# Performance work log

Hardware: AMD Instinct MI355X
Metric: run time of the kernel (lower is better)

The kernel has to match this reference:

```python
import jax, jax.numpy as jnp
import numpy as np
from jax import lax

H = 1024
D = 128
T = 64  # n_step + n_middle


def gru_cell(x, h, w_ih, w_hh, b_ih, b_hh):
    # torch.nn.GRUCell gate order: r, z, n
    gi = x @ w_ih.T + b_ih
    gh = h @ w_hh.T + b_hh
    ir, iz, i_n = jnp.split(gi, 3, axis=-1)
    hr, hz, h_n = jnp.split(gh, 3, axis=-1)
    r = jax.nn.sigmoid(ir + hr)
    z = jax.nn.sigmoid(iz + hz)
    n = jnp.tanh(i_n + r * h_n)
    return (1.0 - z) * n + z * h


def decoder(z_seq, z8, n1, w_init, b_init, wi1, wh1, bi1, bh1, wi2, wh2, bi2, bh2, w_out, b_out):
    B = z_seq.shape[0]
    out0 = jnp.zeros((B, D), z_seq.dtype).at[:, -1].set(1.0)
    h0 = z8 @ w_init.T + b_init              # [B, H]
    h1 = jnp.zeros_like(h0)                  # replaced at i == 0
    xs = (jnp.arange(T), jnp.swapaxes(z_seq, 0, 1))  # ([T], [T, B, D])

    def step(carry, x):
        h0, h1, out = carry
        i, z_i = x
        inp = jnp.where(i <= n1 - 1, z_i, out)
        h0n = gru_cell(inp, h0, wi1, wh1, bi1, bh1)
        h1 = jnp.where(i == 0, h0n, h1)
        h1n = gru_cell(h0n, h1, wi2, wh2, bi2, bh2)
        out = h1n @ w_out.T + b_out          # [B, 128]
        return (h0n, h1n, out), out

    _, outs = lax.scan(step, (h0, h1, out0), xs)  # [T, B, 128]
    return jnp.swapaxes(outs[n1 - 1:], 0, 1)      # [B, T-n1+1, 128]


def _p(key, shape):
    return jax.random.normal(key, shape, dtype=jnp.float32) * 0.02


def setup_inputs() -> dict:
    key = jax.random.key(0)
    ks = jax.random.split(key, 32)
    B = 2048
    inp = {
        'zp': jax.random.normal(ks[0], (B, T, D), jnp.float32),
        'zr': jax.random.normal(ks[1], (B, T, D), jnp.float32),
        'zp8': jax.random.normal(ks[2], (B, D), jnp.float32),
        'zr8': jax.random.normal(ks[3], (B, D), jnp.float32),
        'n1': 16,
        'n2': 48,
    }
    # GRU cells 1..4: (w_ih [3H, in], w_hh [3H, H], b_ih [3H], b_hh [3H])
    for j, name in enumerate(['1', '2', '3', '4']):
        in_dim = D if name in ('1', '3') else H
        inp['wi' + name] = _p(ks[4 + 4 * j], (3 * H, in_dim))
        inp['wh' + name] = _p(ks[5 + 4 * j], (3 * H, H))
        inp['bi' + name] = _p(ks[6 + 4 * j], (3 * H,))
        inp['bh' + name] = _p(ks[7 + 4 * j], (3 * H,))
    inp['w_init0'] = _p(ks[20], (H, D)); inp['b_init0'] = _p(ks[21], (H,))
    inp['w_init1'] = _p(ks[22], (H, D)); inp['b_init1'] = _p(ks[23], (H,))
    inp['w_out0'] = _p(ks[24], (D, H)); inp['b_out0'] = _p(ks[25], (D,))
    inp['w_out1'] = _p(ks[26], (D, H)); inp['b_out1'] = _p(ks[27], (D,))
    return inp


def reference(zp, zr, zp8, zr8, n1, n2,
              wi1, wh1, bi1, bh1, wi2, wh2, bi2, bh2,
              wi3, wh3, bi3, bh3, wi4, wh4, bi4, bh4,
              w_init0, b_init0, w_init1, b_init1,
              w_out0, b_out0, w_out1, b_out1):
    z_r = decoder(zr, zr8, n1, w_init0, b_init0, wi1, wh1, bi1, bh1,
                  wi2, wh2, bi2, bh2, w_out0, b_out0)
    z_p = decoder(zp, zp8, n1, w_init1, b_init1, wi3, wh3, bi3, bh3,
                  wi4, wh4, bi4, bh4, w_out1, b_out1)
    return (z_p, z_r)
```

## Files before the change

kernel.cpp:

```cpp
#include <hip/hip_runtime.h>

typedef unsigned short u16;
typedef unsigned int u32;
typedef __attribute__((ext_vector_type(8))) short short8;
typedef __attribute__((ext_vector_type(4))) float f32x4;

#define DEV __device__ __forceinline__

DEV u16 f2bf(float f){
  u32 u = __builtin_bit_cast(u32, f);
  u += 0x7fffu + ((u >> 16) & 1u);
  return (u16)(u >> 16);
}
DEV float sigm(float x){ return 1.f / (1.f + __expf(-x)); }
DEV float tanh_(float x){ return 2.f / (1.f + __expf(-2.f * x)) - 1.f; }

DEV void gl_lds16(const void* g, void* l){
  __builtin_amdgcn_global_load_lds(
      (const __attribute__((address_space(1))) u32*)g,
      (__attribute__((address_space(3))) u32*)l, 16, 0, 0);
}

__global__ void pack_w_kernel(const float* __restrict__ wi, const float* __restrict__ wh,
                              u16* __restrict__ dst, int Ki, int Kh, int nrows){
  const int KT = Ki + Kh;
  const long n = (long)nrows * KT;
  for (long idx = (long)blockIdx.x * blockDim.x + threadIdx.x; idx < n;
       idx += (long)gridDim.x * blockDim.x){
    int r = (int)(idx / KT), c = (int)(idx % KT);
    float v = (c < Ki) ? wi[(long)r * Ki + c] : wh[(long)r * Kh + (c - Ki)];
    dst[idx] = f2bf(v);
  }
}

struct InitA { const float* z8; const float* wini; const float* bini; float* h0f; u16* h0bf; };

__global__ __launch_bounds__(256)
void init_kernel(InitA A0, InitA A1){
  const InitA& a = (blockIdx.z == 0) ? A0 : A1;
  __shared__ float lz[64][128];
  const int tid = threadIdx.x;
  const int rb = blockIdx.x * 64, ub = blockIdx.y * 128;
  {
    const int row = tid >> 2, q = tid & 3;
    const float4* p = (const float4*)(a.z8 + (long)(rb + row) * 128 + q * 32);
    float4* dst = (float4*)&lz[row][q * 32];
    #pragma unroll
    for (int j = 0; j < 8; ++j) dst[j] = p[j];
  }
  __syncthreads();
  const int u = ub + (tid & 127);
  const int rg = tid >> 7;
  float acc[32];
  #pragma unroll
  for (int r = 0; r < 32; ++r) acc[r] = 0.f;
  for (int k = 0; k < 128; k += 4){
    float4 w4 = *(const float4*)&a.wini[(long)u * 128 + k];
    #pragma unroll
    for (int r = 0; r < 32; ++r){
      float4 z4 = *(const float4*)&lz[rg * 32 + r][k];
      acc[r] += w4.x * z4.x + w4.y * z4.y + w4.z * z4.z + w4.w * z4.w;
    }
  }
  const float b = a.bini[u];
  #pragma unroll
  for (int r = 0; r < 32; ++r){
    const long row = rb + rg * 32 + r;
    const float v = acc[r] + b;
    a.h0f[row * 1024 + u] = v;
    a.h0bf[row * 1024 + u] = f2bf(v);
  }
}

struct CellA {
  const u16* W;
  const float* bi; const float* bh;
  const float* afz; const float* afo;
  const u16* ab1; const u16* ab2;
  const float* holdr; float* holdw; u16* hbfw;
};

template<int CELL>
__global__ __launch_bounds__(256, 2)
void cell_kernel(CellA A0, CellA A1, const int* dn1, int step){
  constexpr int KTOT = (CELL == 1) ? 1152 : 2048;
  constexpr int KT = KTOT / 64;
  constexpr int KSPLIT = (CELL == 1) ? 128 : 1024;

  __shared__ u16 lA[128 * 64];
  __shared__ u16 lB[3][32 * 64];

  const CellA& a = (blockIdx.z == 0) ? A0 : A1;
  const int tid = threadIdx.x;
  const int lane = tid & 63;
  const int wv = tid >> 6;
  const int brow = blockIdx.x * 128;
  const int u0 = blockIdx.y * 32;

  f32x4 accR[2][2] = {}; f32x4 accZ[2][2] = {};
  f32x4 accNI[2][2] = {}; f32x4 accNH[2][2] = {};

  const float* fsrc = nullptr; long fstr = 0;
  if constexpr (CELL == 1){
    const int n1v = *dn1;
    if (step < n1v){ fsrc = a.afz; fstr = 64 * 128; }
    else           { fsrc = a.afo; fstr = 128; }
  }

  const int srow = tid >> 3;
  const int sxor8 = ((tid & 7) ^ (srow & 7)) * 8;

  for (int kt = 0; kt < KT; ++kt){
    const int k0 = kt * 64;
    __syncthreads();
    if constexpr (CELL == 1){
      if (k0 < 128){
        const int row = tid >> 1, half = tid & 1;
        const float* p = fsrc + (long)(brow + row) * fstr + k0 + half * 32;
        #pragma unroll
        for (int q = 0; q < 4; ++q){
          float4 x = ((const float4*)p)[2 * q];
          float4 y = ((const float4*)p)[2 * q + 1];
          short8 o;
          o[0] = (short)f2bf(x.x); o[1] = (short)f2bf(x.y);
          o[2] = (short)f2bf(x.z); o[3] = (short)f2bf(x.w);
          o[4] = (short)f2bf(y.x); o[5] = (short)f2bf(y.y);
          o[6] = (short)f2bf(y.z); o[7] = (short)f2bf(y.w);
          const int s = half * 4 + q;
          *(short8*)&lA[row * 64 + ((s ^ (row & 7)) * 8)] = o;
        }
      } else {
        const int kk = k0 - 128;
        #pragma unroll
        for (int j = 0; j < 4; ++j){
          const int row = j * 32 + srow;
          gl_lds16(a.ab1 + (long)(brow + row) * 1024 + kk + sxor8,
                   &lA[(j * 32 + wv * 8) * 64]);
        }
      }
    } else {
      const u16* ab; int kk;
      if (k0 < 1024){ ab = a.ab1; kk = k0; } else { ab = a.ab2; kk = k0 - 1024; }
      #pragma unroll
      for (int j = 0; j < 4; ++j){
        const int row = j * 32 + srow;
        gl_lds16(ab + (long)(brow + row) * 1024 + kk + sxor8,
                 &lA[(j * 32 + wv * 8) * 64]);
      }
    }
    #pragma unroll
    for (int g = 0; g < 3; ++g){
      gl_lds16(a.W + (long)(g * 1024 + u0 + srow) * KTOT + k0 + sxor8,
               &lB[g][wv * 8 * 64]);
    }
    __syncthreads();

    const int l15 = lane & 15;
    const int kq = lane >> 4;
    const int sx = lane & 7;
    #pragma unroll
    for (int ks = 0; ks < 2; ++ks){
      const int soff = (((ks * 4 + kq) ^ sx)) * 8;
      short8 af[2], bR[2], bZ[2], bN[2];
      #pragma unroll
      for (int fr = 0; fr < 2; ++fr)
        af[fr] = *(const short8*)&lA[(wv * 32 + fr * 16 + l15) * 64 + soff];
      #pragma unroll
      for (int fc = 0; fc < 2; ++fc){
        bR[fc] = *(const short8*)&lB[0][(fc * 16 + l15) * 64 + soff];
        bZ[fc] = *(const short8*)&lB[1][(fc * 16 + l15) * 64 + soff];
        bN[fc] = *(const short8*)&lB[2][(fc * 16 + l15) * 64 + soff];
      }
      if (k0 < KSPLIT){
        #pragma unroll
        for (int fr = 0; fr < 2; ++fr)
          #pragma unroll
          for (int fc = 0; fc < 2; ++fc){
            accR[fr][fc] = __builtin_amdgcn_mfma_f32_16x16x32_bf16(af[fr], bR[fc], accR[fr][fc], 0, 0, 0);
            accZ[fr][fc] = __builtin_amdgcn_mfma_f32_16x16x32_bf16(af[fr], bZ[fc], accZ[fr][fc], 0, 0, 0);
            accNI[fr][fc] = __builtin_amdgcn_mfma_f32_16x16x32_bf16(af[fr], bN[fc], accNI[fr][fc], 0, 0, 0);
          }
      } else {
        #pragma unroll
        for (int fr = 0; fr < 2; ++fr)
          #pragma unroll
          for (int fc = 0; fc < 2; ++fc){
            accR[fr][fc] = __builtin_amdgcn_mfma_f32_16x16x32_bf16(af[fr], bR[fc], accR[fr][fc], 0, 0, 0);
            accZ[fr][fc] = __builtin_amdgcn_mfma_f32_16x16x32_bf16(af[fr], bZ[fc], accZ[fr][fc], 0, 0, 0);
            accNH[fr][fc] = __builtin_amdgcn_mfma_f32_16x16x32_bf16(af[fr], bN[fc], accNH[fr][fc], 0, 0, 0);
          }
      }
    }
  }

  const int l15 = lane & 15;
  const int rq = (lane >> 4) * 4;
  #pragma unroll
  for (int fc = 0; fc < 2; ++fc){
    const int u = u0 + fc * 16 + l15;
    const float br = a.bi[u] + a.bh[u];
    const float bz = a.bi[1024 + u] + a.bh[1024 + u];
    const float bni = a.bi[2048 + u];
    const float bnh = a.bh[2048 + u];
    #pragma unroll
    for (int fr = 0; fr < 2; ++fr){
      #pragma unroll
      for (int rg = 0; rg < 4; ++rg){
        const long row = brow + wv * 32 + fr * 16 + rq + rg;
        const float r = sigm(accR[fr][fc][rg] + br);
        const float z = sigm(accZ[fr][fc][rg] + bz);
        const float n = tanh_(accNI[fr][fc][rg] + bni + r * (accNH[fr][fc][rg] + bnh));
        const float hp = a.holdr[row * 1024 + u];
        const float hn = (1.f - z) * n + z * hp;
        a.holdw[row * 1024 + u] = hn;
        a.hbfw[row * 1024 + u] = f2bf(hn);
      }
    }
  }
}

struct OutA { const u16* Ah; const u16* Wo; const float* bo; float* outf; };

__global__ __launch_bounds__(256, 2)
void out_kernel(OutA A0, OutA A1, const int* dn1, int step, float* __restrict__ dout, long outhalf){
  const int n1v = *dn1;
  if (step < n1v - 1) return;
  __shared__ u16 lA[32 * 64];
  __shared__ u16 lB[128 * 64];
  const OutA& a = (blockIdx.z == 0) ? A0 : A1;
  const int tid = threadIdx.x, lane = tid & 63, wv = tid >> 6;
  const int brow = blockIdx.x * 32;
  f32x4 acc[2][2] = {};
  const int srow = tid >> 3;
  const int sxor8 = ((tid & 7) ^ (srow & 7)) * 8;

  for (int kt = 0; kt < 16; ++kt){
    const int k0 = kt * 64;
    __syncthreads();
    gl_lds16(a.Ah + (long)(brow + srow) * 1024 + k0 + sxor8, &lA[wv * 8 * 64]);
    #pragma unroll
    for (int j = 0; j < 4; ++j){
      const int row = j * 32 + srow;
      gl_lds16(a.Wo + (long)row * 1024 + k0 + sxor8, &lB[(j * 32 + wv * 8) * 64]);
    }
    __syncthreads();
    const int l15 = lane & 15, kq = lane >> 4, sx = lane & 7;
    #pragma unroll
    for (int ks = 0; ks < 2; ++ks){
      const int soff = (((ks * 4 + kq) ^ sx)) * 8;
      short8 af[2], bf[2];
      af[0] = *(const short8*)&lA[(l15) * 64 + soff];
      af[1] = *(const short8*)&lA[(16 + l15) * 64 + soff];
      bf[0] = *(const short8*)&lB[(wv * 32 + l15) * 64 + soff];
      bf[1] = *(const short8*)&lB[(wv * 32 + 16 + l15) * 64 + soff];
      #pragma unroll
      for (int fr = 0; fr < 2; ++fr)
        #pragma unroll
        for (int fc = 0; fc < 2; ++fc)
          acc[fr][fc] = __builtin_amdgcn_mfma_f32_16x16x32_bf16(af[fr], bf[fc], acc[fr][fc], 0, 0, 0);
    }
  }
  const int nst = 65 - n1v;
  const int t = step - (n1v - 1);
  const int l15 = lane & 15;
  const int rq = (lane >> 4) * 4;
  #pragma unroll
  for (int fc = 0; fc < 2; ++fc){
    const int u = wv * 32 + fc * 16 + l15;
    const float bo = a.bo[u];
    #pragma unroll
    for (int fr = 0; fr < 2; ++fr){
      #pragma unroll
      for (int rg = 0; rg < 4; ++rg){
        const long row = brow + fr * 16 + rq + rg;
        const float v = acc[fr][fc][rg] + bo;
        a.outf[row * 128 + u] = v;
        dout[(long)blockIdx.z * outhalf + (row * nst + t) * 128 + u] = v;
      }
    }
  }
}

extern "C" void kernel_launch(void* const* d_in, const int* in_sizes, int n_in,
                              void* d_out, int out_size, void* d_ws, size_t ws_size,
                              hipStream_t stream){
  const float* zz[2]   = { (const float*)d_in[0],  (const float*)d_in[1] };
  const float* z8[2]   = { (const float*)d_in[2],  (const float*)d_in[3] };
  const int* dn1       = (const int*)d_in[4];
  const float* wi_c1[2] = { (const float*)d_in[14], (const float*)d_in[6] };
  const float* wh_c1[2] = { (const float*)d_in[15], (const float*)d_in[7] };
  const float* bi_c1[2] = { (const float*)d_in[16], (const float*)d_in[8] };
  const float* bh_c1[2] = { (const float*)d_in[17], (const float*)d_in[9] };
  const float* wi_c2[2] = { (const float*)d_in[18], (const float*)d_in[10] };
  const float* wh_c2[2] = { (const float*)d_in[19], (const float*)d_in[11] };
  const float* bi_c2[2] = { (const float*)d_in[20], (const float*)d_in[12] };
  const float* bh_c2[2] = { (const float*)d_in[21], (const float*)d_in[13] };
  const float* wini[2]  = { (const float*)d_in[24], (const float*)d_in[22] };
  const float* bini[2]  = { (const float*)d_in[25], (const float*)d_in[23] };
  const float* wout[2]  = { (const float*)d_in[28], (const float*)d_in[26] };
  const float* bout[2]  = { (const float*)d_in[29], (const float*)d_in[27] };

  char* p = (char*)d_ws;
  auto alloc = [&](size_t bytes)->char*{
    char* q = p; p += (bytes + 255) & ~(size_t)255; return q;
  };
  u16* W1c[2]; u16* W2c[2]; u16* Woc[2];
  float* h0f[2]; float* h1f[2]; float* outf[2];
  u16* h0bf[2][2]; u16* h1bf[2][2];
  for (int d = 0; d < 2; ++d){
    W1c[d] = (u16*)alloc(3072ULL * 1152 * 2);
    W2c[d] = (u16*)alloc(3072ULL * 2048 * 2);
    Woc[d] = (u16*)alloc(128ULL * 1024 * 2);
    h0f[d] = (float*)alloc(2048ULL * 1024 * 4);
    h1f[d] = (float*)alloc(2048ULL * 1024 * 4);
    outf[d] = (float*)alloc(2048ULL * 128 * 4);
    for (int b = 0; b < 2; ++b){
      h0bf[d][b] = (u16*)alloc(2048ULL * 1024 * 2);
      h1bf[d][b] = (u16*)alloc(2048ULL * 1024 * 2);
    }
  }
  if ((size_t)(p - (char*)d_ws) > ws_size) return;

  for (int d = 0; d < 2; ++d){
    pack_w_kernel<<<dim3(1024), dim3(256), 0, stream>>>(wi_c1[d], wh_c1[d], W1c[d], 128, 1024, 3072);
    pack_w_kernel<<<dim3(1024), dim3(256), 0, stream>>>(wi_c2[d], wh_c2[d], W2c[d], 1024, 1024, 3072);
    pack_w_kernel<<<dim3(64),   dim3(256), 0, stream>>>(wout[d], wout[d], Woc[d], 1024, 0, 128);
  }
  {
    InitA I0{ z8[0], wini[0], bini[0], h0f[0], h0bf[0][0] };
    InitA I1{ z8[1], wini[1], bini[1], h0f[1], h0bf[1][0] };
    init_kernel<<<dim3(32, 8, 2), dim3(256), 0, stream>>>(I0, I1);
  }

  const long outhalf = (long)out_size / 2;

  for (int i = 0; i < 64; ++i){
    const int cur = i & 1, nxt = cur ^ 1;
    CellA c1[2], c2[2];
    for (int d = 0; d < 2; ++d){
      c1[d] = CellA{ W1c[d], bi_c1[d], bh_c1[d],
                     zz[d] + (long)i * 128, outf[d],
                     h0bf[d][cur], nullptr,
                     h0f[d], h0f[d], h0bf[d][nxt] };
      c2[d] = CellA{ W2c[d], bi_c2[d], bh_c2[d],
                     nullptr, nullptr,
                     h0bf[d][nxt], (i == 0) ? h0bf[d][nxt] : h1bf[d][cur],
                     (i == 0) ? h0f[d] : h1f[d], h1f[d], h1bf[d][nxt] };
    }
    cell_kernel<1><<<dim3(16, 32, 2), dim3(256), 0, stream>>>(c1[0], c1[1], dn1, i);
    cell_kernel<2><<<dim3(16, 32, 2), dim3(256), 0, stream>>>(c2[0], c2[1], dn1, i);
    OutA o0{ h1bf[0][nxt], Woc[0], bout[0], outf[0] };
    OutA o1{ h1bf[1][nxt], Woc[1], bout[1], outf[1] };
    out_kernel<<<dim3(64, 1, 2), dim3(256), 0, stream>>>(o0, o1, dn1, i, (float*)d_out, outhalf);
  }
}
```

Measured before the change: 8.247 ms.

## Double-buffer LDS tiles in GRU cell and output GEMM kernels

Both the GRU cell kernel and the output projection kernel now keep two LDS buffers. The next K-tile's global-to-LDS loads are issued before the MFMA work on the current tile, with one barrier per iteration instead of two. This is meant to hide global load latency behind compute. It doubles shared memory use, which may lower occupancy under launch_bounds(256,2), and relies on the async global_load_lds having completed by the time of the barrier.

```diff
diff --git a/kernel.cpp b/kernel.cpp
--- a/kernel.cpp
+++ b/kernel.cpp
@@ -87,8 +87,8 @@
   constexpr int KT = KTOT / 64;
   constexpr int KSPLIT = (CELL == 1) ? 128 : 1024;
 
-  __shared__ u16 lA[128 * 64];
-  __shared__ u16 lB[3][32 * 64];
+  __shared__ u16 lA[2][128 * 64];
+  __shared__ u16 lB[2][3][32 * 64];
 
   const CellA& a = (blockIdx.z == 0) ? A0 : A1;
   const int tid = threadIdx.x;
@@ -110,9 +110,8 @@
   const int srow = tid >> 3;
   const int sxor8 = ((tid & 7) ^ (srow & 7)) * 8;
 
-  for (int kt = 0; kt < KT; ++kt){
+  auto stage = [&](int bf, int kt){
     const int k0 = kt * 64;
-    __syncthreads();
     if constexpr (CELL == 1){
       if (k0 < 128){
         const int row = tid >> 1, half = tid & 1;
@@ -127,7 +126,7 @@
           o[4] = (short)f2bf(y.x); o[5] = (short)f2bf(y.y);
           o[6] = (short)f2bf(y.z); o[7] = (short)f2bf(y.w);
           const int s = half * 4 + q;
-          *(short8*)&lA[row * 64 + ((s ^ (row & 7)) * 8)] = o;
+          *(short8*)&lA[bf][row * 64 + ((s ^ (row & 7)) * 8)] = o;
         }
       } else {
         const int kk = k0 - 128;
@@ -135,7 +134,7 @@
         for (int j = 0; j < 4; ++j){
           const int row = j * 32 + srow;
           gl_lds16(a.ab1 + (long)(brow + row) * 1024 + kk + sxor8,
-                   &lA[(j * 32 + wv * 8) * 64]);
+                   &lA[bf][(j * 32 + wv * 8) * 64]);
         }
       }
     } else {
@@ -145,16 +144,23 @@
       for (int j = 0; j < 4; ++j){
         const int row = j * 32 + srow;
         gl_lds16(ab + (long)(brow + row) * 1024 + kk + sxor8,
-                 &lA[(j * 32 + wv * 8) * 64]);
+                 &lA[bf][(j * 32 + wv * 8) * 64]);
       }
     }
     #pragma unroll
     for (int g = 0; g < 3; ++g){
       gl_lds16(a.W + (long)(g * 1024 + u0 + srow) * KTOT + k0 + sxor8,
-               &lB[g][wv * 8 * 64]);
-    }
-    __syncthreads();
-
+               &lB[bf][g][wv * 8 * 64]);
+    }
+  };
+
+  stage(0, 0);
+  __syncthreads();
+  int buf = 0;
+  for (int kt = 0; kt < KT; ++kt){
+    if (kt + 1 < KT) stage(buf ^ 1, kt + 1);
+
+    const int k0 = kt * 64;
     const int l15 = lane & 15;
     const int kq = lane >> 4;
     const int sx = lane & 7;
@@ -164,12 +170,12 @@
       short8 af[2], bR[2], bZ[2], bN[2];
       #pragma unroll
       for (int fr = 0; fr < 2; ++fr)
-        af[fr] = *(const short8*)&lA[(wv * 32 + fr * 16 + l15) * 64 + soff];
+        af[fr] = *(const short8*)&lA[buf][(wv * 32 + fr * 16 + l15) * 64 + soff];
       #pragma unroll
       for (int fc = 0; fc < 2; ++fc){
-        bR[fc] = *(const short8*)&lB[0][(fc * 16 + l15) * 64 + soff];
-        bZ[fc] = *(const short8*)&lB[1][(fc * 16 + l15) * 64 + soff];
-        bN[fc] = *(const short8*)&lB[2][(fc * 16 + l15) * 64 + soff];
+        bR[fc] = *(const short8*)&lB[buf][0][(fc * 16 + l15) * 64 + soff];
+        bZ[fc] = *(const short8*)&lB[buf][1][(fc * 16 + l15) * 64 + soff];
+        bN[fc] = *(const short8*)&lB[buf][2][(fc * 16 + l15) * 64 + soff];
       }
       if (k0 < KSPLIT){
         #pragma unroll
@@ -191,6 +197,8 @@
           }
       }
     }
+
+    if (kt + 1 < KT){ __syncthreads(); buf ^= 1; }
   }
 
   const int l15 = lane & 15;
@@ -225,8 +233,8 @@
 void out_kernel(OutA A0, OutA A1, const int* dn1, int step, float* __restrict__ dout, long outhalf){
   const int n1v = *dn1;
   if (step < n1v - 1) return;
-  __shared__ u16 lA[32 * 64];
-  __shared__ u16 lB[128 * 64];
+  __shared__ u16 lA[2][32 * 64];
+  __shared__ u16 lB[2][128 * 64];
   const OutA& a = (blockIdx.z == 0) ? A0 : A1;
   const int tid = threadIdx.x, lane = tid & 63, wv = tid >> 6;
   const int brow = blockIdx.x * 32;
@@ -234,31 +242,37 @@
   const int srow = tid >> 3;
   const int sxor8 = ((tid & 7) ^ (srow & 7)) * 8;
 
-  for (int kt = 0; kt < 16; ++kt){
+  auto stage = [&](int bf, int kt){
     const int k0 = kt * 64;
-    __syncthreads();
-    gl_lds16(a.Ah + (long)(brow + srow) * 1024 + k0 + sxor8, &lA[wv * 8 * 64]);
+    gl_lds16(a.Ah + (long)(brow + srow) * 1024 + k0 + sxor8, &lA[bf][wv * 8 * 64]);
     #pragma unroll
     for (int j = 0; j < 4; ++j){
       const int row = j * 32 + srow;
-      gl_lds16(a.Wo + (long)row * 1024 + k0 + sxor8, &lB[(j * 32 + wv * 8) * 64]);
-    }
-    __syncthreads();
+      gl_lds16(a.Wo + (long)row * 1024 + k0 + sxor8, &lB[bf][(j * 32 + wv * 8) * 64]);
+    }
+  };
+
+  stage(0, 0);
+  __syncthreads();
+  int buf = 0;
+  for (int kt = 0; kt < 16; ++kt){
+    if (kt + 1 < 16) stage(buf ^ 1, kt + 1);
     const int l15 = lane & 15, kq = lane >> 4, sx = lane & 7;
     #pragma unroll
     for (int ks = 0; ks < 2; ++ks){
       const int soff = (((ks * 4 + kq) ^ sx)) * 8;
-      short8 af[2], bf[2];
-      af[0] = *(const short8*)&lA[(l15) * 64 + soff];
-      af[1] = *(const short8*)&lA[(16 + l15) * 64 + soff];
-      bf[0] = *(const short8*)&lB[(wv * 32 + l15) * 64 + soff];
-      bf[1] = *(const short8*)&lB[(wv * 32 + 16 + l15) * 64 + soff];
+      short8 af[2], bf2[2];
+      af[0] = *(const short8*)&lA[buf][(l15) * 64 + soff];
+      af[1] = *(const short8*)&lA[buf][(16 + l15) * 64 + soff];
+      bf2[0] = *(const short8*)&lB[buf][(wv * 32 + l15) * 64 + soff];
+      bf2[1] = *(const short8*)&lB[buf][(wv * 32 + 16 + l15) * 64 + soff];
       #pragma unroll
       for (int fr = 0; fr < 2; ++fr)
         #pragma unroll
         for (int fc = 0; fc < 2; ++fc)
-          acc[fr][fc] = __builtin_amdgcn_mfma_f32_16x16x32_bf16(af[fr], bf[fc], acc[fr][fc], 0, 0, 0);
-    }
+          acc[fr][fc] = __builtin_amdgcn_mfma_f32_16x16x32_bf16(af[fr], bf2[fc], acc[fr][fc], 0, 0, 0);
+    }
+    if (kt + 1 < 16){ __syncthreads(); buf ^= 1; }
   }
   const int nst = 65 - n1v;
   const int t = step - (n1v - 1);
```

Result: slower. 8.857 ms (+7.4%).
